# Performance work log

Measured on AMD Instinct MI355X. Metric: run time of the kernel, lower is better.

Reference implementation:

```python
import jax, jax.numpy as jnp
import numpy as np

H = 256  # LSTM hidden units per layer

def _cell(xt, h, c, W, U, b):
    # Keras LSTMCell: gate order i, f, g(cell), o; sigmoid recurrent activation, tanh activation
    z = xt @ W + h @ U + b  # (B, 4H)
    i, f, g, o = jnp.split(z, 4, axis=-1)
    c_new = jax.nn.sigmoid(f) * c + jax.nn.sigmoid(i) * jnp.tanh(g)
    h_new = jax.nn.sigmoid(o) * jnp.tanh(c_new)
    return h_new, c_new

def _stacked_lstm(x, W1, U1, b1, W2, U2, b2):
    # x: (B, T, F). Returns concat of FINAL CELL STATES of both layers: (B, 2H)
    # (original code takes outputs[i+1][1], i.e. the c state of each LSTMCell)
    B = x.shape[0]
    def step(carry, xt):
        h1, c1, h2, c2 = carry
        h1, c1 = _cell(xt, h1, c1, W1, U1, b1)
        h2, c2 = _cell(h1, h2, c2, W2, U2, b2)
        return (h1, c1, h2, c2), None
    z0 = jnp.zeros((B, H), x.dtype)
    (h1, c1, h2, c2), _ = jax.lax.scan(step, (z0, z0, z0, z0), jnp.swapaxes(x, 0, 1))
    return jnp.concatenate([c1, c2], axis=-1)

def _glorot(key, shape):
    lim = np.sqrt(6.0 / (shape[0] + shape[1]))
    return jax.random.uniform(key, shape, jnp.float32, -lim, lim)

def _lstm_bias():
    # Keras unit_forget_bias=True: forget-gate bias initialized to 1
    return jnp.zeros((4 * H,), jnp.float32).at[H:2 * H].set(1.0)

def setup_inputs():
    key = jax.random.key(0)
    ks = jax.random.split(key, 16)
    B, T, F, ZD = 16384, 20, 80, 32
    inp = {
        "x": jax.random.normal(ks[0], (B, T, F), jnp.float32),
        "eps1": jax.random.normal(ks[1], (B, ZD), jnp.float32),
        "eps2": jax.random.normal(ks[2], (B, ZD), jnp.float32),
        # z2 stacked LSTM (input F)
        "z2_W1": _glorot(ks[3], (F, 4 * H)), "z2_U1": _glorot(ks[4], (H, 4 * H)), "z2_b1": _lstm_bias(),
        "z2_W2": _glorot(ks[5], (H, 4 * H)), "z2_U2": _glorot(ks[6], (H, 4 * H)), "z2_b2": _lstm_bias(),
        # z1 stacked LSTM (input F + z2_dim)
        "z1_W1": _glorot(ks[7], (F + ZD, 4 * H)), "z1_U1": _glorot(ks[8], (H, 4 * H)), "z1_b1": _lstm_bias(),
        "z1_W2": _glorot(ks[9], (H, 4 * H)), "z1_U2": _glorot(ks[10], (H, 4 * H)), "z1_b2": _lstm_bias(),
        # dense heads (input 2H -> ZD), linear (mu_nl=logvar_nl=None)
        "mu2_W": _glorot(ks[11], (2 * H, ZD)), "mu2_b": jnp.zeros((ZD,), jnp.float32),
        "lv2_W": _glorot(ks[12], (2 * H, ZD)), "lv2_b": jnp.zeros((ZD,), jnp.float32),
        "mu1_W": _glorot(ks[13], (2 * H, ZD)), "mu1_b": jnp.zeros((ZD,), jnp.float32),
        "lv1_W": _glorot(ks[14], (2 * H, ZD)), "lv1_b": jnp.zeros((ZD,), jnp.float32),
    }
    return inp

def reference(x, eps1, eps2,
              z2_W1, z2_U1, z2_b1, z2_W2, z2_U2, z2_b2,
              z1_W1, z1_U1, z1_b1, z1_W2, z1_U2, z1_b2,
              mu2_W, mu2_b, lv2_W, lv2_b, mu1_W, mu1_b, lv1_W, lv1_b):
    B, T, _ = x.shape
    # z2 branch
    z2_pre = _stacked_lstm(x, z2_W1, z2_U1, z2_b1, z2_W2, z2_U2, z2_b2)  # (B, 2H)
    z2_mu = z2_pre @ mu2_W + mu2_b
    z2_logvar = z2_pre @ lv2_W + lv2_b
    z2_sample = eps2 * jnp.exp(0.5 * z2_logvar) + z2_mu  # reparameterize
    # z1 branch: tile z2_sample over time, concat with x
    z2_tiled = jnp.broadcast_to(z2_sample[:, None, :], (B, T, z2_sample.shape[-1]))
    x_z2 = jnp.concatenate([x, z2_tiled], axis=-1)  # (B, T, F+ZD)
    z1_pre = _stacked_lstm(x_z2, z1_W1, z1_U1, z1_b1, z1_W2, z1_U2, z1_b2)
    z1_mu = z1_pre @ mu1_W + mu1_b
    z1_logvar = z1_pre @ lv1_W + lv1_b
    z1_sample = eps1 * jnp.exp(0.5 * z1_logvar) + z1_mu
    return (z1_mu, z1_logvar, z1_sample, z2_mu, z2_logvar, z2_sample)
```

## Files before the change

kernel.cpp:

```cpp
#include <hip/hip_runtime.h>
#include <hip/hip_bf16.h>

#define B_SZ 16384
#define T_SZ 20

typedef __attribute__((ext_vector_type(8))) __bf16 bf16x8;
typedef __attribute__((ext_vector_type(4))) float f32x4;

__device__ __forceinline__ float sigm(float x){ return 1.f/(1.f+__expf(-x)); }
__device__ __forceinline__ float tanh_(float x){ return 1.f-2.f/(__expf(2.f*x)+1.f); }

#define OFF_L1Z2 0
#define OFF_L2Z2 360448
#define OFF_L1Z1 884736
#define OFF_L2Z1 1277952
#define OFF_HZ2  1802240
#define OFF_HZ1  1835008
#define WP_TOT   1867776

__global__ void prep_w(const float* __restrict__ W0, const float* __restrict__ U0,
                       const float* __restrict__ W1, const float* __restrict__ U1,
                       const float* __restrict__ W2, const float* __restrict__ U2,
                       const float* __restrict__ W3, const float* __restrict__ U3,
                       const float* __restrict__ muW2, const float* __restrict__ lvW2,
                       const float* __restrict__ muW1, const float* __restrict__ lvW1,
                       __bf16* __restrict__ wp)
{
    int idx = blockIdx.x * 256 + threadIdx.x;
    if (idx >= WP_TOT) return;
    if (idx < OFF_HZ2) {
        const float *W, *U;
        int Fx, Kx, KT, local;
        if (idx < OFF_L2Z2)      { W = W0; U = U0; Fx = 80;  Kx = 96;  KT = 11; local = idx; }
        else if (idx < OFF_L1Z1) { W = W1; U = U1; Fx = 256; Kx = 256; KT = 16; local = idx - OFF_L2Z2; }
        else if (idx < OFF_L2Z1) { W = W2; U = U2; Fx = 112; Kx = 128; KT = 12; local = idx - OFF_L1Z1; }
        else                     { W = W3; U = U3; Fx = 256; Kx = 256; KT = 16; local = idx - OFF_L2Z1; }
        int jj = local & 7, lane = (local >> 3) & 63, nt8 = (local >> 9) & 7, rest = local >> 12;
        int kt = rest % KT, wgn = rest / KT;
        int gate = nt8 >> 1, hh = nt8 & 1;
        int n = gate * 256 + wgn * 32 + hh * 16 + (lane & 15);
        int k = kt * 32 + ((lane >> 4) << 3) + jj;
        float v = (k < Fx) ? W[k * 1024 + n] : (k < Kx ? 0.f : U[(k - Kx) * 1024 + n]);
        wp[idx] = (__bf16)v;
    } else {
        int base = (idx < OFF_HZ1) ? OFF_HZ2 : OFF_HZ1;
        const float* mw = (idx < OFF_HZ1) ? muW2 : muW1;
        const float* lw = (idx < OFF_HZ1) ? lvW2 : lvW1;
        int local = idx - base;
        int jj = local & 7, lane = (local >> 3) & 63, nt = (local >> 9) & 3, kt = local >> 11;
        int k = kt * 32 + ((lane >> 4) << 3) + jj;
        int c16 = lane & 15;
        float v = (nt < 2) ? mw[k * 32 + nt * 16 + c16] : lw[k * 32 + (nt - 2) * 16 + c16];
        wp[idx] = (__bf16)v;
    }
}

__device__ __forceinline__ void stage16(const __bf16* g, __bf16* l)
{
    __builtin_amdgcn_global_load_lds(
        (const __attribute__((address_space(1))) unsigned*)g,
        (__attribute__((address_space(3))) unsigned*)l, 16, 0, 0);
}

template <int HASZ>
__device__ __forceinline__ bf16x8 xfrag(const float* __restrict__ x, const __bf16* __restrict__ z2b,
                                        int row, int t, int k)
{
    bf16x8 r;
    if (k < 80) {
        const float4* p = reinterpret_cast<const float4*>(x + ((size_t)row * T_SZ + t) * 80 + k);
        float4 u0 = p[0], u1 = p[1];
        r[0] = (__bf16)u0.x; r[1] = (__bf16)u0.y; r[2] = (__bf16)u0.z; r[3] = (__bf16)u0.w;
        r[4] = (__bf16)u1.x; r[5] = (__bf16)u1.y; r[6] = (__bf16)u1.z; r[7] = (__bf16)u1.w;
    } else if (HASZ && k < 112) {
        r = *reinterpret_cast<const bf16x8*>(z2b + (size_t)row * 32 + (k - 80));
    } else {
#pragma unroll
        for (int i = 0; i < 8; ++i) r[i] = (__bf16)0.f;
    }
    return r;
}

template <int MODE>
__global__ void __launch_bounds__(512, 4)
step_gemm(const float* __restrict__ x, const __bf16* __restrict__ z2b, int t,
          const __bf16* __restrict__ hA, const __bf16* __restrict__ hB,
          const __bf16* __restrict__ wpm, const float* __restrict__ bias,
          float* __restrict__ cbuf, __bf16* __restrict__ hout)
{
    constexpr int KT  = (MODE == 0) ? 11 : (MODE == 1) ? 12 : 16;
    constexpr int XKT = (MODE == 0) ? 3  : (MODE == 1) ? 4  : 0;
    constexpr int P   = (KT + 1) / 2;
    __shared__ __align__(16) __bf16 Bs[4][4096];

    const int tid = threadIdx.x;
    const int w = tid >> 6, lane = tid & 63;
    const int r16 = lane & 15, kq = lane >> 4;
    const int mid = blockIdx.x & 63, wgn = blockIdx.x >> 6;
    const int rb = mid * 256 + w * 32;
    const __bf16* wpB = wpm + (size_t)wgn * KT * 4096;

    f32x4 acc[8][2];
#pragma unroll
    for (int nt = 0; nt < 8; ++nt)
#pragma unroll
        for (int m = 0; m < 2; ++m) acc[nt][m] = f32x4{0.f, 0.f, 0.f, 0.f};

    auto do_kt = [&](int kt) {
        bf16x8 a0, a1;
        if (MODE < 2 && kt < XKT) {
            int k = kt * 32 + kq * 8;
            a0 = xfrag<MODE == 1>(x, z2b, rb + r16, t, k);
            a1 = xfrag<MODE == 1>(x, z2b, rb + 16 + r16, t, k);
        } else {
            const __bf16* hs;
            int hk;
            if (MODE < 2)    { hs = hA; hk = (kt - XKT) * 32 + kq * 8; }
            else if (kt < 8) { hs = hA; hk = kt * 32 + kq * 8; }
            else             { hs = hB; hk = (kt - 8) * 32 + kq * 8; }
            hs += (size_t)(rb + r16) * 256 + hk;
            a0 = *reinterpret_cast<const bf16x8*>(hs);
            a1 = *reinterpret_cast<const bf16x8*>(hs + 16 * 256);
        }
        const __bf16* bp = &Bs[kt & 3][lane * 8];
#pragma unroll
        for (int nt = 0; nt < 8; ++nt) {
            bf16x8 bv = *reinterpret_cast<const bf16x8*>(bp + nt * 512);
            acc[nt][0] = __builtin_amdgcn_mfma_f32_16x16x32_bf16(a0, bv, acc[nt][0], 0, 0, 0);
            acc[nt][1] = __builtin_amdgcn_mfma_f32_16x16x32_bf16(a1, bv, acc[nt][1], 0, 0, 0);
        }
    };

    stage16(wpB + tid * 8, &Bs[0][tid * 8]);
    stage16(wpB + 4096 + tid * 8, &Bs[1][tid * 8]);
    __syncthreads();

#pragma unroll
    for (int p = 0; p < P; ++p) {
        const int ks = 2 * p + 2;
        if (ks < KT)     stage16(wpB + (size_t)ks * 4096 + tid * 8, &Bs[ks & 3][tid * 8]);
        if (ks + 1 < KT) stage16(wpB + (size_t)(ks + 1) * 4096 + tid * 8, &Bs[(ks + 1) & 3][tid * 8]);
        do_kt(2 * p);
        if (2 * p + 1 < KT) do_kt(2 * p + 1);
        __syncthreads();
    }

    float bg[2][4];
#pragma unroll
    for (int hh = 0; hh < 2; ++hh)
#pragma unroll
        for (int gate = 0; gate < 4; ++gate)
            bg[hh][gate] = bias[gate * 256 + wgn * 32 + hh * 16 + r16];

#pragma unroll
    for (int m = 0; m < 2; ++m)
#pragma unroll
        for (int hh = 0; hh < 2; ++hh) {
            const int hcol = wgn * 32 + hh * 16 + r16;
            f32x4 zi = acc[0 + hh][m], zf = acc[2 + hh][m], zg = acc[4 + hh][m], zo = acc[6 + hh][m];
#pragma unroll
            for (int q = 0; q < 4; ++q) {
                int row = rb + m * 16 + kq * 4 + q;
                size_t off = (size_t)row * 256 + hcol;
                float co = cbuf[off];
                float cn = sigm(zf[q] + bg[hh][1]) * co
                         + sigm(zi[q] + bg[hh][0]) * tanh_(zg[q] + bg[hh][2]);
                cbuf[off] = cn;
                hout[off] = (__bf16)(sigm(zo[q] + bg[hh][3]) * tanh_(cn));
            }
        }
}

__global__ void __launch_bounds__(128, 4)
head_mfma(const float* __restrict__ c1, const float* __restrict__ c2,
          const __bf16* __restrict__ hp, const float* __restrict__ mub,
          const float* __restrict__ lvb, const float* __restrict__ eps,
          float* __restrict__ omu, float* __restrict__ olv, float* __restrict__ osm,
          __bf16* __restrict__ osb)
{
    const int tid = threadIdx.x;
    const int w = tid >> 6, lane = tid & 63;
    const int r16 = lane & 15, kq = lane >> 4;
    const int rb = blockIdx.x * 64 + w * 32;

    f32x4 acc[4][2];
#pragma unroll
    for (int nt = 0; nt < 4; ++nt)
#pragma unroll
        for (int m = 0; m < 2; ++m) acc[nt][m] = f32x4{0.f, 0.f, 0.f, 0.f};

#pragma unroll
    for (int kt = 0; kt < 16; ++kt) {
        const float* cs = (kt < 8) ? c1 : c2;
        int k = (kt & 7) * 32 + kq * 8;
        bf16x8 a[2];
#pragma unroll
        for (int m = 0; m < 2; ++m) {
            const float* pr = cs + (size_t)(rb + m * 16 + r16) * 256 + k;
            float4 u0 = reinterpret_cast<const float4*>(pr)[0];
            float4 u1 = reinterpret_cast<const float4*>(pr)[1];
            a[m][0] = (__bf16)u0.x; a[m][1] = (__bf16)u0.y; a[m][2] = (__bf16)u0.z; a[m][3] = (__bf16)u0.w;
            a[m][4] = (__bf16)u1.x; a[m][5] = (__bf16)u1.y; a[m][6] = (__bf16)u1.z; a[m][7] = (__bf16)u1.w;
        }
        const __bf16* hb = hp + kt * 2048 + lane * 8;
#pragma unroll
        for (int nt = 0; nt < 4; ++nt) {
            bf16x8 bv = *reinterpret_cast<const bf16x8*>(hb + nt * 512);
            acc[nt][0] = __builtin_amdgcn_mfma_f32_16x16x32_bf16(a[0], bv, acc[nt][0], 0, 0, 0);
            acc[nt][1] = __builtin_amdgcn_mfma_f32_16x16x32_bf16(a[1], bv, acc[nt][1], 0, 0, 0);
        }
    }

#pragma unroll
    for (int m = 0; m < 2; ++m)
#pragma unroll
        for (int q = 0; q < 4; ++q) {
            int row = rb + m * 16 + kq * 4 + q;
#pragma unroll
            for (int z = 0; z < 2; ++z) {
                int zc = z * 16 + r16;
                float mu = acc[z][m][q] + mub[zc];
                float lv = acc[z + 2][m][q] + lvb[zc];
                int idx = row * 32 + zc;
                omu[idx] = mu;
                olv[idx] = lv;
                float s = fmaf(eps[idx], expf(0.5f * lv), mu);
                osm[idx] = s;
                if (osb) osb[idx] = (__bf16)s;
            }
        }
}

extern "C" void kernel_launch(void* const* d_in, const int* in_sizes, int n_in,
                              void* d_out, int out_size, void* d_ws, size_t ws_size,
                              hipStream_t stream)
{
    const float* x    = (const float*)d_in[0];
    const float* eps1 = (const float*)d_in[1];
    const float* eps2 = (const float*)d_in[2];
    const float* z2W1 = (const float*)d_in[3];
    const float* z2U1 = (const float*)d_in[4];
    const float* z2b1 = (const float*)d_in[5];
    const float* z2W2 = (const float*)d_in[6];
    const float* z2U2 = (const float*)d_in[7];
    const float* z2b2 = (const float*)d_in[8];
    const float* z1W1 = (const float*)d_in[9];
    const float* z1U1 = (const float*)d_in[10];
    const float* z1b1 = (const float*)d_in[11];
    const float* z1W2 = (const float*)d_in[12];
    const float* z1U2 = (const float*)d_in[13];
    const float* z1b2 = (const float*)d_in[14];
    const float* mu2W = (const float*)d_in[15];
    const float* mu2b = (const float*)d_in[16];
    const float* lv2W = (const float*)d_in[17];
    const float* lv2b = (const float*)d_in[18];
    const float* mu1W = (const float*)d_in[19];
    const float* mu1b = (const float*)d_in[20];
    const float* lv1W = (const float*)d_in[21];
    const float* lv1b = (const float*)d_in[22];

    char* ws = (char*)d_ws;
    __bf16* wp   = (__bf16*)ws;
    __bf16* z2sb = (__bf16*)(ws + 4194304);
    __bf16* h1a  = (__bf16*)(ws + 5242880);
    __bf16* h2a  = (__bf16*)(ws + 13631488);
    __bf16* h1b  = (__bf16*)(ws + 22020096);
    __bf16* h2b  = (__bf16*)(ws + 30408704);
    float*  c1   = (float*)(ws + 38797312);
    float*  c2   = (float*)(ws + 55574528);

    __bf16* h1[2] = {h1a, h1b};
    __bf16* h2[2] = {h2a, h2b};

    float* out = (float*)d_out;
    const int BZ = B_SZ * 32;
    float* z1mu = out;           float* z1lv = out + BZ;     float* z1sm = out + 2 * BZ;
    float* z2mu = out + 3 * BZ;  float* z2lv = out + 4 * BZ; float* z2sm = out + 5 * BZ;

    prep_w<<<7296, 256, 0, stream>>>(z2W1, z2U1, z2W2, z2U2, z1W1, z1U1, z1W2, z1U2,
                                     mu2W, lv2W, mu1W, lv1W, wp);

    hipMemsetAsync(ws + 22020096, 0, 50331648, stream);
    for (int t = 0; t < T_SZ; ++t) {
        int cur = t & 1, prv = cur ^ 1;
        step_gemm<0><<<512, 512, 0, stream>>>(x, nullptr, t, h1[prv], nullptr,
                                              wp + OFF_L1Z2, z2b1, c1, h1[cur]);
        step_gemm<2><<<512, 512, 0, stream>>>(nullptr, nullptr, t, h1[cur], h2[prv],
                                              wp + OFF_L2Z2, z2b2, c2, h2[cur]);
    }
    head_mfma<<<256, 128, 0, stream>>>(c1, c2, wp + OFF_HZ2, mu2b, lv2b, eps2,
                                       z2mu, z2lv, z2sm, z2sb);

    hipMemsetAsync(ws + 22020096, 0, 50331648, stream);
    for (int t = 0; t < T_SZ; ++t) {
        int cur = t & 1, prv = cur ^ 1;
        step_gemm<1><<<512, 512, 0, stream>>>(x, z2sb, t, h1[prv], nullptr,
                                              wp + OFF_L1Z1, z1b1, c1, h1[cur]);
        step_gemm<2><<<512, 512, 0, stream>>>(nullptr, nullptr, t, h1[cur], h2[prv],
                                              wp + OFF_L2Z1, z1b2, c2, h2[cur]);
    }
    head_mfma<<<256, 128, 0, stream>>>(c1, c2, wp + OFF_HZ1, mu1b, lv1b, eps1,
                                       z1mu, z1lv, z1sm, nullptr);
}
```

Measured before the change: 2.509 ms.

## Pre-convert inputs to bf16, prefetch A fragments, skip zero-state work at t=0

Converts x to a padded bf16 buffer once and broadcasts the z2 sample into it, so each step no longer converts fp32 inputs. Step kernels now use 256-thread blocks with 128-row tiles and 1024 blocks. A-operand loads are double-buffered in registers so the next fragment loads while the current MFMAs run. The t=0 step is specialised to skip the zero hidden-state K tiles and the forget-gate term, which removes the memsets. This costs an extra 84MB workspace and more register pressure.

```diff
diff --git a/kernel.cpp b/kernel.cpp
--- a/kernel.cpp
+++ b/kernel.cpp
@@ -55,6 +55,33 @@
     }
 }
 
+__global__ void xconv(const float* __restrict__ x, __bf16* __restrict__ xb)
+{
+    int idx = blockIdx.x * 256 + threadIdx.x;
+    int c8 = idx & 15, row = idx >> 4;
+    bf16x8 r;
+    if (c8 < 10) {
+        const float4* p = reinterpret_cast<const float4*>(x + (size_t)row * 80 + c8 * 8);
+        float4 u0 = p[0], u1 = p[1];
+        r[0]=(__bf16)u0.x; r[1]=(__bf16)u0.y; r[2]=(__bf16)u0.z; r[3]=(__bf16)u0.w;
+        r[4]=(__bf16)u1.x; r[5]=(__bf16)u1.y; r[6]=(__bf16)u1.z; r[7]=(__bf16)u1.w;
+    } else {
+#pragma unroll
+        for (int i = 0; i < 8; ++i) r[i] = (__bf16)0.f;
+    }
+    *reinterpret_cast<bf16x8*>(xb + (size_t)row * 128 + c8 * 8) = r;
+}
+
+__global__ void bcast_z2(const __bf16* __restrict__ z2sb, __bf16* __restrict__ xb)
+{
+    int idx = blockIdx.x * 256 + threadIdx.x;
+    int g = idx & 3, b = idx >> 2;
+    bf16x8 v = *reinterpret_cast<const bf16x8*>(z2sb + (size_t)b * 32 + g * 8);
+#pragma unroll
+    for (int t = 0; t < T_SZ; ++t)
+        *reinterpret_cast<bf16x8*>(xb + ((size_t)b * T_SZ + t) * 128 + 80 + g * 8) = v;
+}
+
 __device__ __forceinline__ void stage16(const __bf16* g, __bf16* l)
 {
     __builtin_amdgcn_global_load_lds(
@@ -62,43 +89,32 @@
         (__attribute__((address_space(3))) unsigned*)l, 16, 0, 0);
 }
 
-template <int HASZ>
-__device__ __forceinline__ bf16x8 xfrag(const float* __restrict__ x, const __bf16* __restrict__ z2b,
-                                        int row, int t, int k)
-{
-    bf16x8 r;
-    if (k < 80) {
-        const float4* p = reinterpret_cast<const float4*>(x + ((size_t)row * T_SZ + t) * 80 + k);
-        float4 u0 = p[0], u1 = p[1];
-        r[0] = (__bf16)u0.x; r[1] = (__bf16)u0.y; r[2] = (__bf16)u0.z; r[3] = (__bf16)u0.w;
-        r[4] = (__bf16)u1.x; r[5] = (__bf16)u1.y; r[6] = (__bf16)u1.z; r[7] = (__bf16)u1.w;
-    } else if (HASZ && k < 112) {
-        r = *reinterpret_cast<const bf16x8*>(z2b + (size_t)row * 32 + (k - 80));
-    } else {
-#pragma unroll
-        for (int i = 0; i < 8; ++i) r[i] = (__bf16)0.f;
-    }
-    return r;
-}
-
-template <int MODE>
-__global__ void __launch_bounds__(512, 4)
-step_gemm(const float* __restrict__ x, const __bf16* __restrict__ z2b, int t,
+template <int KT, int KTP, int XKT, int TWOH, int FIRST>
+__global__ void __launch_bounds__(256, 4)
+step_gemm(const __bf16* __restrict__ xb, int t,
           const __bf16* __restrict__ hA, const __bf16* __restrict__ hB,
           const __bf16* __restrict__ wpm, const float* __restrict__ bias,
           float* __restrict__ cbuf, __bf16* __restrict__ hout)
 {
-    constexpr int KT  = (MODE == 0) ? 11 : (MODE == 1) ? 12 : 16;
-    constexpr int XKT = (MODE == 0) ? 3  : (MODE == 1) ? 4  : 0;
-    constexpr int P   = (KT + 1) / 2;
+    constexpr int P = (KT + 1) / 2;
     __shared__ __align__(16) __bf16 Bs[4][4096];
 
     const int tid = threadIdx.x;
     const int w = tid >> 6, lane = tid & 63;
     const int r16 = lane & 15, kq = lane >> 4;
-    const int mid = blockIdx.x & 63, wgn = blockIdx.x >> 6;
-    const int rb = mid * 256 + w * 32;
-    const __bf16* wpB = wpm + (size_t)wgn * KT * 4096;
+    const int mid = blockIdx.x & 127, wgn = blockIdx.x >> 7;
+    const int rb = mid * 128 + w * 32;
+    const __bf16* wpB = wpm + (size_t)wgn * KTP * 4096;
+
+    const __bf16 *x0 = nullptr, *x1 = nullptr;
+    if (XKT > 0) {
+        x0 = xb + ((size_t)(rb + r16) * T_SZ + t) * 128;
+        x1 = xb + ((size_t)(rb + 16 + r16) * T_SZ + t) * 128;
+    }
+    const __bf16* hA0 = hA + (size_t)(rb + r16) * 256;
+    const __bf16* hA1 = hA + (size_t)(rb + 16 + r16) * 256;
+    const __bf16* hB0 = TWOH ? hB + (size_t)(rb + r16) * 256 : nullptr;
+    const __bf16* hB1 = TWOH ? hB + (size_t)(rb + 16 + r16) * 256 : nullptr;
 
     f32x4 acc[8][2];
 #pragma unroll
@@ -106,42 +122,59 @@
 #pragma unroll
         for (int m = 0; m < 2; ++m) acc[nt][m] = f32x4{0.f, 0.f, 0.f, 0.f};
 
-    auto do_kt = [&](int kt) {
-        bf16x8 a0, a1;
-        if (MODE < 2 && kt < XKT) {
-            int k = kt * 32 + kq * 8;
-            a0 = xfrag<MODE == 1>(x, z2b, rb + r16, t, k);
-            a1 = xfrag<MODE == 1>(x, z2b, rb + 16 + r16, t, k);
-        } else {
-            const __bf16* hs;
-            int hk;
-            if (MODE < 2)    { hs = hA; hk = (kt - XKT) * 32 + kq * 8; }
-            else if (kt < 8) { hs = hA; hk = kt * 32 + kq * 8; }
-            else             { hs = hB; hk = (kt - 8) * 32 + kq * 8; }
-            hs += (size_t)(rb + r16) * 256 + hk;
-            a0 = *reinterpret_cast<const bf16x8*>(hs);
-            a1 = *reinterpret_cast<const bf16x8*>(hs + 16 * 256);
-        }
-        const __bf16* bp = &Bs[kt & 3][lane * 8];
-#pragma unroll
-        for (int nt = 0; nt < 8; ++nt) {
-            bf16x8 bv = *reinterpret_cast<const bf16x8*>(bp + nt * 512);
-            acc[nt][0] = __builtin_amdgcn_mfma_f32_16x16x32_bf16(a0, bv, acc[nt][0], 0, 0, 0);
-            acc[nt][1] = __builtin_amdgcn_mfma_f32_16x16x32_bf16(a1, bv, acc[nt][1], 0, 0, 0);
-        }
+    auto aptr = [&](int kt, int m) -> const __bf16* {
+        if (kt < XKT) return (m ? x1 : x0) + kt * 32 + kq * 8;
+        int kk = kt - XKT;
+        if (!TWOH || kk < 8) return (m ? hA1 : hA0) + kk * 32 + kq * 8;
+        return (m ? hB1 : hB0) + (kk - 8) * 32 + kq * 8;
     };
-
-    stage16(wpB + tid * 8, &Bs[0][tid * 8]);
-    stage16(wpB + 4096 + tid * 8, &Bs[1][tid * 8]);
+    auto loadPh = [&](int k0, bf16x8* a) {
+        a[0] = *reinterpret_cast<const bf16x8*>(aptr(k0, 0));
+        a[1] = *reinterpret_cast<const bf16x8*>(aptr(k0, 1));
+        if (k0 + 1 < KT) {
+            a[2] = *reinterpret_cast<const bf16x8*>(aptr(k0 + 1, 0));
+            a[3] = *reinterpret_cast<const bf16x8*>(aptr(k0 + 1, 1));
+        }
+    };
+    auto compPh = [&](int k0, const bf16x8* a) {
+        {
+            const __bf16* bp = &Bs[k0 & 3][lane * 8];
+#pragma unroll
+            for (int nt = 0; nt < 8; ++nt) {
+                bf16x8 bv = *reinterpret_cast<const bf16x8*>(bp + nt * 512);
+                acc[nt][0] = __builtin_amdgcn_mfma_f32_16x16x32_bf16(a[0], bv, acc[nt][0], 0, 0, 0);
+                acc[nt][1] = __builtin_amdgcn_mfma_f32_16x16x32_bf16(a[1], bv, acc[nt][1], 0, 0, 0);
+            }
+        }
+        if (k0 + 1 < KT) {
+            const __bf16* bp = &Bs[(k0 + 1) & 3][lane * 8];
+#pragma unroll
+            for (int nt = 0; nt < 8; ++nt) {
+                bf16x8 bv = *reinterpret_cast<const bf16x8*>(bp + nt * 512);
+                acc[nt][0] = __builtin_amdgcn_mfma_f32_16x16x32_bf16(a[2], bv, acc[nt][0], 0, 0, 0);
+                acc[nt][1] = __builtin_amdgcn_mfma_f32_16x16x32_bf16(a[3], bv, acc[nt][1], 0, 0, 0);
+            }
+        }
+    };
+    auto stageKt = [&](int kt) {
+        const __bf16* g = wpB + (size_t)kt * 4096 + tid * 8;
+        stage16(g, &Bs[kt & 3][tid * 8]);
+        stage16(g + 2048, &Bs[kt & 3][2048 + tid * 8]);
+    };
+
+    bf16x8 aP[2][4];
+    stageKt(0);
+    if (KT > 1) stageKt(1);
+    loadPh(0, aP[0]);
     __syncthreads();
 
 #pragma unroll
     for (int p = 0; p < P; ++p) {
         const int ks = 2 * p + 2;
-        if (ks < KT)     stage16(wpB + (size_t)ks * 4096 + tid * 8, &Bs[ks & 3][tid * 8]);
-        if (ks + 1 < KT) stage16(wpB + (size_t)(ks + 1) * 4096 + tid * 8, &Bs[(ks + 1) & 3][tid * 8]);
-        do_kt(2 * p);
-        if (2 * p + 1 < KT) do_kt(2 * p + 1);
+        if (ks < KT)     stageKt(ks);
+        if (ks + 1 < KT) stageKt(ks + 1);
+        if (ks < KT)     loadPh(ks, aP[(p + 1) & 1]);
+        compPh(2 * p, aP[p & 1]);
         __syncthreads();
     }
 
@@ -162,9 +195,14 @@
             for (int q = 0; q < 4; ++q) {
                 int row = rb + m * 16 + kq * 4 + q;
                 size_t off = (size_t)row * 256 + hcol;
-                float co = cbuf[off];
-                float cn = sigm(zf[q] + bg[hh][1]) * co
-                         + sigm(zi[q] + bg[hh][0]) * tanh_(zg[q] + bg[hh][2]);
+                float cn;
+                if (FIRST) {
+                    cn = sigm(zi[q] + bg[hh][0]) * tanh_(zg[q] + bg[hh][2]);
+                } else {
+                    float co = cbuf[off];
+                    cn = sigm(zf[q] + bg[hh][1]) * co
+                       + sigm(zi[q] + bg[hh][0]) * tanh_(zg[q] + bg[hh][2]);
+                }
                 cbuf[off] = cn;
                 hout[off] = (__bf16)(sigm(zo[q] + bg[hh][3]) * tanh_(cn));
             }
@@ -199,8 +237,8 @@
             const float* pr = cs + (size_t)(rb + m * 16 + r16) * 256 + k;
             float4 u0 = reinterpret_cast<const float4*>(pr)[0];
             float4 u1 = reinterpret_cast<const float4*>(pr)[1];
-            a[m][0] = (__bf16)u0.x; a[m][1] = (__bf16)u0.y; a[m][2] = (__bf16)u0.z; a[m][3] = (__bf16)u0.w;
-            a[m][4] = (__bf16)u1.x; a[m][5] = (__bf16)u1.y; a[m][6] = (__bf16)u1.z; a[m][7] = (__bf16)u1.w;
+            a[m][0]=(__bf16)u0.x; a[m][1]=(__bf16)u0.y; a[m][2]=(__bf16)u0.z; a[m][3]=(__bf16)u0.w;
+            a[m][4]=(__bf16)u1.x; a[m][5]=(__bf16)u1.y; a[m][6]=(__bf16)u1.z; a[m][7]=(__bf16)u1.w;
         }
         const __bf16* hb = hp + kt * 2048 + lane * 8;
 #pragma unroll
@@ -262,12 +300,13 @@
     char* ws = (char*)d_ws;
     __bf16* wp   = (__bf16*)ws;
     __bf16* z2sb = (__bf16*)(ws + 4194304);
-    __bf16* h1a  = (__bf16*)(ws + 5242880);
-    __bf16* h2a  = (__bf16*)(ws + 13631488);
-    __bf16* h1b  = (__bf16*)(ws + 22020096);
-    __bf16* h2b  = (__bf16*)(ws + 30408704);
-    float*  c1   = (float*)(ws + 38797312);
-    float*  c2   = (float*)(ws + 55574528);
+    __bf16* xb   = (__bf16*)(ws + 5242880);
+    __bf16* h1a  = (__bf16*)(ws + 89128960);
+    __bf16* h2a  = (__bf16*)(ws + 97517568);
+    __bf16* h1b  = (__bf16*)(ws + 105906176);
+    __bf16* h2b  = (__bf16*)(ws + 114294784);
+    float*  c1   = (float*)(ws + 122683392);
+    float*  c2   = (float*)(ws + 139460608);
 
     __bf16* h1[2] = {h1a, h1b};
     __bf16* h2[2] = {h2a, h2b};
@@ -277,27 +316,35 @@
     float* z1mu = out;           float* z1lv = out + BZ;     float* z1sm = out + 2 * BZ;
     float* z2mu = out + 3 * BZ;  float* z2lv = out + 4 * BZ; float* z2sm = out + 5 * BZ;
 
+    xconv<<<B_SZ * T_SZ * 16 / 256, 256, 0, stream>>>(x, xb);
     prep_w<<<7296, 256, 0, stream>>>(z2W1, z2U1, z2W2, z2U2, z1W1, z1U1, z1W2, z1U2,
                                      mu2W, lv2W, mu1W, lv1W, wp);
 
-    hipMemsetAsync(ws + 22020096, 0, 50331648, stream);
-    for (int t = 0; t < T_SZ; ++t) {
+    step_gemm<3, 11, 3, 0, 1><<<1024, 256, 0, stream>>>(xb, 0, h1a, nullptr,
+                                                        wp + OFF_L1Z2, z2b1, c1, h1[0]);
+    step_gemm<8, 16, 0, 1, 1><<<1024, 256, 0, stream>>>(xb, 0, h1[0], h2a,
+                                                        wp + OFF_L2Z2, z2b2, c2, h2[0]);
+    for (int t = 1; t < T_SZ; ++t) {
         int cur = t & 1, prv = cur ^ 1;
-        step_gemm<0><<<512, 512, 0, stream>>>(x, nullptr, t, h1[prv], nullptr,
-                                              wp + OFF_L1Z2, z2b1, c1, h1[cur]);
-        step_gemm<2><<<512, 512, 0, stream>>>(nullptr, nullptr, t, h1[cur], h2[prv],
-                                              wp + OFF_L2Z2, z2b2, c2, h2[cur]);
+        step_gemm<11, 11, 3, 0, 0><<<1024, 256, 0, stream>>>(xb, t, h1[prv], nullptr,
+                                                             wp + OFF_L1Z2, z2b1, c1, h1[cur]);
+        step_gemm<16, 16, 0, 1, 0><<<1024, 256, 0, stream>>>(xb, t, h1[cur], h2[prv],
+                                                             wp + OFF_L2Z2, z2b2, c2, h2[cur]);
     }
     head_mfma<<<256, 128, 0, stream>>>(c1, c2, wp + OFF_HZ2, mu2b, lv2b, eps2,
                                        z2mu, z2lv, z2sm, z2sb);
-
-    hipMemsetAsync(ws + 22020096, 0, 50331648, stream);
-    for (int t = 0; t < T_SZ; ++t) {
+    bcast_z2<<<B_SZ * 4 / 256, 256, 0, stream>>>(z2sb, xb);
+
+    step_gemm<4, 12, 4, 0, 1><<<1024, 256, 0, stream>>>(xb, 0, h1a, nullptr,
+                                                        wp + OFF_L1Z1, z1b1, c1, h1[0]);
+    step_gemm<8, 16, 0, 1, 1><<<1024, 256, 0, stream>>>(xb, 0, h1[0], h2a,
+                                                        wp + OFF_L2Z1, z1b2, c2, h2[0]);
+    for (int t = 1; t < T_SZ; ++t) {
         int cur = t & 1, prv = cur ^ 1;
-        step_gemm<1><<<512, 512, 0, stream>>>(x, z2sb, t, h1[prv], nullptr,
-                                              wp + OFF_L1Z1, z1b1, c1, h1[cur]);
-        step_gemm<2><<<512, 512, 0, stream>>>(nullptr, nullptr, t, h1[cur], h2[prv],
-                                              wp + OFF_L2Z1, z1b2, c2, h2[cur]);
+        step_gemm<12, 12, 4, 0, 0><<<1024, 256, 0, stream>>>(xb, t, h1[prv], nullptr,
+                                                             wp + OFF_L1Z1, z1b1, c1, h1[cur]);
+        step_gemm<16, 16, 0, 1, 0><<<1024, 256, 0, stream>>>(xb, t, h1[cur], h2[prv],
+                                                             wp + OFF_L2Z1, z1b2, c2, h2[cur]);
     }
     head_mfma<<<256, 128, 0, stream>>>(c1, c2, wp + OFF_HZ1, mu1b, lv1b, eps1,
                                        z1mu, z1lv, z1sm, nullptr);
```

Result: faster. 2.373 ms (-5.4%).
